# Optimization experiments

Measured on AMD Instinct MI355X. Metric: run time of the kernel, lower is better.

## Reference

```python
import jax, jax.numpy as jnp
import numpy as np

N = 50000      # nodes
DEG = 16       # in-degree per node -> E = 800k edges
IN = 256       # in_size
HID = 32       # hid_size
HEAD = 4       # heads in first layer
OUT = 40       # out_size (classes)
HH = HID * HEAD  # 128, hidden width
NEG_SLOPE = 0.2


def setup_inputs() -> dict:
    key = jax.random.key(0)
    ks = jax.random.split(key, 16)
    E = N * DEG
    src = jax.random.randint(ks[0], (E,), 0, N)
    dst = jnp.repeat(jnp.arange(N), DEG)  # every node has DEG in-edges

    def nrm(k, shape):
        return jax.random.normal(k, shape, jnp.float32) * 0.1

    return dict(
        features=jax.random.normal(ks[1], (N, IN), jnp.float32),
        src=src, dst=dst,
        # layer 1: GATConv(IN -> HID, HEAD heads)
        W1=nrm(ks[2], (IN, HH)), al1=nrm(ks[3], (HEAD, HID)), ar1=nrm(ks[4], (HEAD, HID)), b1=nrm(ks[5], (HH,)),
        # hidden layer: GATConv(HH -> HH, 1 head)
        Wh=nrm(ks[6], (HH, HH)), alh=nrm(ks[7], (1, HH)), arh=nrm(ks[8], (1, HH)), bh=nrm(ks[9], (HH,)),
        # layer 2: GATConv(HH -> OUT, 1 head)
        W2=nrm(ks[10], (HH, OUT)), al2=nrm(ks[11], (1, OUT)), ar2=nrm(ks[12], (1, OUT)), b2=nrm(ks[13], (OUT,)),
    )


def gat_conv(x, src, dst, W, al, ar, b):
    """DGL-style GATConv. x:[N,F], W:[F,H*D], al/ar:[H,D], b:[H*D]. Returns [N,H,D]."""
    n = x.shape[0]
    H, D = al.shape
    feat = (x @ W).reshape(n, H, D)                 # [N,H,D]
    el = jnp.sum(feat * al, axis=-1)                # [N,H]
    er = jnp.sum(feat * ar, axis=-1)                # [N,H]
    e = jax.nn.leaky_relu(el[src] + er[dst], NEG_SLOPE)  # [E,H] per-edge logits
    # segment softmax over each destination's in-edges
    emax = jax.lax.stop_gradient(jax.ops.segment_max(e, dst, num_segments=n))  # [N,H]
    ex = jnp.exp(e - emax[dst])                     # [E,H]
    den = jax.ops.segment_sum(ex, dst, num_segments=n)  # [N,H]
    alpha = ex / den[dst]                           # [E,H]
    out = jax.ops.segment_sum(feat[src] * alpha[:, :, None], dst, num_segments=n)  # [N,H,D]
    return out + b.reshape(1, H, D)


def reference(features, src, dst, W1, al1, ar1, b1, Wh, alh, arh, bh, W2, al2, ar2, b2):
    # conv1 -> flatten heads -> relu
    h = jax.nn.relu(gat_conv(features, src, dst, W1, al1, ar1, b1).reshape(N, HH))
    # hidden GATConv (1 head) -> mean over head -> relu (dropout is identity in eval)
    h = jax.nn.relu(gat_conv(h, src, dst, Wh, alh, arh, bh).mean(axis=1))
    # conv2 (1 head) -> mean over head -> log_softmax
    h = gat_conv(h, src, dst, W2, al2, ar2, b2).mean(axis=1)
    return jax.nn.log_softmax(h, axis=1)
```

## Files before the change

### kernel.cpp

```cpp
#include <hip/hip_runtime.h>
#include <cstddef>
#include <math.h>

#define NN 50000
#define DEG 16
#define NEG_SLOPE 0.2f

typedef __attribute__((ext_vector_type(8))) short bf16x8;
typedef __attribute__((ext_vector_type(4))) float f32x4;

__device__ inline unsigned short f2bf(float x) {
    unsigned u = __float_as_uint(x);
    return (unsigned short)((u + 0x7FFF + ((u >> 16) & 1)) >> 16);
}
__device__ inline float bf2f(unsigned short u) {
    return __uint_as_float(((unsigned)u) << 16);
}
__device__ inline unsigned pack_bf2(float lo, float hi) {
    return (unsigned)f2bf(lo) | ((unsigned)f2bf(hi) << 16);
}
__device__ inline void gld_lds16f(const float* g, float* l) {
    __builtin_amdgcn_global_load_lds((const __attribute__((address_space(1))) void*)g,
                                     (__attribute__((address_space(3))) void*)l, 16, 0, 0);
}

__global__ void prep_k(const float* __restrict__ W1, unsigned short* __restrict__ Wt1,
                       const float* __restrict__ Wh, unsigned short* __restrict__ Wth)
{
    const int b = blockIdx.x;
    if (b < 128) {
        int idx = b * 256 + threadIdx.x;
        int c = idx >> 8, k = idx & 255;
        Wt1[idx] = f2bf(W1[(size_t)k * 128 + c]);
    } else {
        int idx = (b - 128) * 256 + threadIdx.x;
        int c = idx >> 7, k = idx & 127;
        Wth[idx] = f2bf(Wh[(size_t)k * 128 + c]);
    }
}

__launch_bounds__(256)
__global__ void gemm1_k(const float* __restrict__ A,
                        const unsigned short* __restrict__ Wt,
                        const float* __restrict__ al, const float* __restrict__ ar,
                        unsigned short* __restrict__ feat,
                        float* __restrict__ el, float* __restrict__ er)
{
    constexpr int K = 256, KS = 8, TPB = 4;
    __shared__ __align__(16) float buf[2][4096];
    const int tid = threadIdx.x;
    const int w = tid >> 6, l = tid & 63;
    const int lr = l & 15, lq = l >> 4;
    const int col0 = w * 32;

    bf16x8 B0[KS], B1[KS];
#pragma unroll
    for (int ks = 0; ks < KS; ks++) {
        B0[ks] = *(const bf16x8*)(Wt + (size_t)(col0 + lr) * K + ks * 32 + lq * 8);
        B1[ks] = *(const bf16x8*)(Wt + (size_t)(col0 + 16 + lr) * K + ks * 32 + lq * 8);
    }

    const int t0 = blockIdx.x * TPB;
    const int tmax = NN / 16;
    const int t1 = (t0 + TPB < tmax) ? t0 + TPB : tmax;
    if (t0 >= tmax) return;

    auto stage = [&](int t, int b) {
#pragma unroll
        for (int p = 0; p < 4; p++) {
            int j = tid + p * 256;
            int row = j >> 6;
            int kg = (j & 63) ^ (row & 7);
            gld_lds16f(A + (size_t)(t * 16 + row) * 256 + kg * 4, &buf[b][(size_t)j * 4]);
        }
    };
    stage(t0, t0 & 1);

    for (int t = t0; t < t1; ++t) {
        __syncthreads();
        if (t + 1 < t1) stage(t + 1, (t + 1) & 1);

        f32x4 acc0 = {0.f, 0.f, 0.f, 0.f}, acc1 = {0.f, 0.f, 0.f, 0.f};
        const float* bb = buf[t & 1];
#pragma unroll
        for (int ks = 0; ks < KS; ks++) {
            const int kg0 = ks * 8 + lq * 2;
            const int s0 = lr * 64 + (kg0 ^ (lr & 7));
            const int s1 = lr * 64 + ((kg0 + 1) ^ (lr & 7));
            float4 va = *(const float4*)&bb[(size_t)s0 * 4];
            float4 vb = *(const float4*)&bb[(size_t)s1 * 4];
            bf16x8 a = {(short)f2bf(va.x), (short)f2bf(va.y),
                        (short)f2bf(va.z), (short)f2bf(va.w),
                        (short)f2bf(vb.x), (short)f2bf(vb.y),
                        (short)f2bf(vb.z), (short)f2bf(vb.w)};
            acc0 = __builtin_amdgcn_mfma_f32_16x16x32_bf16(a, B0[ks], acc0, 0, 0, 0);
            acc1 = __builtin_amdgcn_mfma_f32_16x16x32_bf16(a, B1[ks], acc1, 0, 0, 0);
        }

        const int row0 = t * 16;
#pragma unroll
        for (int reg = 0; reg < 4; reg++) {
            const int r = row0 + lq * 4 + reg;
            feat[(size_t)r * 128 + col0 + lr]      = f2bf(acc0[reg]);
            feat[(size_t)r * 128 + col0 + 16 + lr] = f2bf(acc1[reg]);
        }

        float pe[4], pr[4];
#pragma unroll
        for (int reg = 0; reg < 4; reg++) {
            pe[reg] = acc0[reg] * al[col0 + lr] + acc1[reg] * al[col0 + 16 + lr];
            pr[reg] = acc0[reg] * ar[col0 + lr] + acc1[reg] * ar[col0 + 16 + lr];
        }
#pragma unroll
        for (int m = 1; m < 16; m <<= 1)
#pragma unroll
            for (int reg = 0; reg < 4; reg++) {
                pe[reg] += __shfl_xor(pe[reg], m);
                pr[reg] += __shfl_xor(pr[reg], m);
            }
        if (lr == 0) {
#pragma unroll
            for (int reg = 0; reg < 4; reg++) {
                const int r = row0 + lq * 4 + reg;
                el[r * 4 + w] = pe[reg];
                er[r * 4 + w] = pr[reg];
            }
        }
    }
}

__launch_bounds__(256)
__global__ void fusedh_k(const unsigned short* __restrict__ feat1,
                         const float* __restrict__ el1, const float* __restrict__ er1,
                         const int* __restrict__ src, const float* __restrict__ b1,
                         const unsigned short* __restrict__ Wt,
                         const float* __restrict__ alh, const float* __restrict__ arh,
                         unsigned short* __restrict__ feat2,
                         float* __restrict__ el, float* __restrict__ er)
{
    __shared__ __align__(16) unsigned short abuf[256 * 8];
    __shared__ float s_alpha[16][64];
    __shared__ float redE[4][16], redR[4][16];
    const int tid = threadIdx.x;
    const int w = tid >> 6, lane = tid & 63;
    const int q = lane >> 4, li = lane & 15;
    const int slot = w * 4 + q;
    const int row0 = blockIdx.x * 16;
    const int node = row0 + slot;
    const int col0 = w * 32;

    const int s = src[node * DEG + li];
    {
        const float4 elv = *(const float4*)(el1 + (size_t)s * 4);
        const float4 erv = *(const float4*)(er1 + (size_t)node * 4);
        float e[4] = {elv.x + erv.x, elv.y + erv.y, elv.z + erv.z, elv.w + erv.w};
#pragma unroll
        for (int h = 0; h < 4; h++) {
            float x = e[h];
            x = (x > 0.f) ? x : NEG_SLOPE * x;
            float mx = x;
#pragma unroll
            for (int d = 1; d < 16; d <<= 1) mx = fmaxf(mx, __shfl_xor(mx, d, 16));
            float ex = expf(x - mx);
            float den = ex;
#pragma unroll
            for (int d = 1; d < 16; d <<= 1) den += __shfl_xor(den, d, 16);
            s_alpha[slot][h * 16 + li] = ex / den;
        }
    }
    uint4 v[16];
#pragma unroll
    for (int jj = 0; jj < 16; jj++) {
        int sj = __shfl(s, (lane & 48) | jj);
        v[jj] = *(const uint4*)(feat1 + (size_t)sj * 128 + li * 8);
    }
    float acc[8] = {0.f, 0.f, 0.f, 0.f, 0.f, 0.f, 0.f, 0.f};
    const int hrow = (li >> 2) * 16;
#pragma unroll
    for (int jj = 0; jj < 16; jj++) {
        float a = s_alpha[slot][hrow + jj];
        unsigned u0 = v[jj].x, u1 = v[jj].y, u2 = v[jj].z, u3 = v[jj].w;
        acc[0] += a * bf2f((unsigned short)(u0 & 0xFFFF));
        acc[1] += a * bf2f((unsigned short)(u0 >> 16));
        acc[2] += a * bf2f((unsigned short)(u1 & 0xFFFF));
        acc[3] += a * bf2f((unsigned short)(u1 >> 16));
        acc[4] += a * bf2f((unsigned short)(u2 & 0xFFFF));
        acc[5] += a * bf2f((unsigned short)(u2 >> 16));
        acc[6] += a * bf2f((unsigned short)(u3 & 0xFFFF));
        acc[7] += a * bf2f((unsigned short)(u3 >> 16));
    }
    const float4 bb0 = *(const float4*)(b1 + li * 8);
    const float4 bb1 = *(const float4*)(b1 + li * 8 + 4);
    float o[8];
    o[0] = fmaxf(acc[0] + bb0.x, 0.f); o[1] = fmaxf(acc[1] + bb0.y, 0.f);
    o[2] = fmaxf(acc[2] + bb0.z, 0.f); o[3] = fmaxf(acc[3] + bb0.w, 0.f);
    o[4] = fmaxf(acc[4] + bb1.x, 0.f); o[5] = fmaxf(acc[5] + bb1.y, 0.f);
    o[6] = fmaxf(acc[6] + bb1.z, 0.f); o[7] = fmaxf(acc[7] + bb1.w, 0.f);
    {
        uint4 pk;
        pk.x = pack_bf2(o[0], o[1]);
        pk.y = pack_bf2(o[2], o[3]);
        pk.z = pack_bf2(o[4], o[5]);
        pk.w = pack_bf2(o[6], o[7]);
        int jw = ((li >> 2) * 64 + (li & 3) * 16 + slot) ^ (li & 7);
        *(uint4*)&abuf[(size_t)jw * 8] = pk;
    }

    bf16x8 B0[4], B1[4];
#pragma unroll
    for (int ks = 0; ks < 4; ks++) {
        B0[ks] = *(const bf16x8*)(Wt + (size_t)(col0 + li) * 128 + ks * 32 + q * 8);
        B1[ks] = *(const bf16x8*)(Wt + (size_t)(col0 + 16 + li) * 128 + ks * 32 + q * 8);
    }
    __syncthreads();

    f32x4 acc0 = {0.f, 0.f, 0.f, 0.f}, acc1 = {0.f, 0.f, 0.f, 0.f};
#pragma unroll
    for (int ks = 0; ks < 4; ks++) {
        int jr = (ks * 64 + lane) ^ ((ks * 4 + q) & 7);
        bf16x8 a = *(const bf16x8*)&abuf[(size_t)jr * 8];
        acc0 = __builtin_amdgcn_mfma_f32_16x16x32_bf16(a, B0[ks], acc0, 0, 0, 0);
        acc1 = __builtin_amdgcn_mfma_f32_16x16x32_bf16(a, B1[ks], acc1, 0, 0, 0);
    }

#pragma unroll
    for (int reg = 0; reg < 4; reg++) {
        const int r = row0 + q * 4 + reg;
        feat2[(size_t)r * 128 + col0 + li]      = f2bf(acc0[reg]);
        feat2[(size_t)r * 128 + col0 + 16 + li] = f2bf(acc1[reg]);
    }
    float pe[4], pr[4];
#pragma unroll
    for (int reg = 0; reg < 4; reg++) {
        pe[reg] = acc0[reg] * alh[col0 + li] + acc1[reg] * alh[col0 + 16 + li];
        pr[reg] = acc0[reg] * arh[col0 + li] + acc1[reg] * arh[col0 + 16 + li];
    }
#pragma unroll
    for (int m = 1; m < 16; m <<= 1)
#pragma unroll
        for (int reg = 0; reg < 4; reg++) {
            pe[reg] += __shfl_xor(pe[reg], m);
            pr[reg] += __shfl_xor(pr[reg], m);
        }
    if (li == 0) {
#pragma unroll
        for (int reg = 0; reg < 4; reg++) {
            redE[w][q * 4 + reg] = pe[reg];
            redR[w][q * 4 + reg] = pr[reg];
        }
    }
    __syncthreads();
    if (tid < 16) {
        el[row0 + tid] = redE[0][tid] + redE[1][tid] + redE[2][tid] + redE[3][tid];
        er[row0 + tid] = redR[0][tid] + redR[1][tid] + redR[2][tid] + redR[3][tid];
    }
}

__launch_bounds__(256)
__global__ void fused40_k(const unsigned short* __restrict__ feat2,
                          const float* __restrict__ elA, const float* __restrict__ erA,
                          const int* __restrict__ src, const float* __restrict__ bh,
                          const float* __restrict__ W2,
                          const float* __restrict__ al2, const float* __restrict__ ar2,
                          unsigned short* __restrict__ f40,
                          float* __restrict__ el2, float* __restrict__ er2)
{
    __shared__ float As[32][132];
    __shared__ float Ws[128 * 40];
    const int tid = threadIdx.x;
    const int w = tid >> 6, lane = tid & 63;
    const int q = lane >> 4, li = lane & 15;
    const int slot = w * 4 + q;
    const int row0 = blockIdx.x * 32;

#pragma unroll
    for (int rnd = 0; rnd < 2; rnd++) {
        const int row = rnd * 16 + slot;
        int node = row0 + row;
        if (node > NN - 1) node = NN - 1;
        const int s = src[node * DEG + li];
        float x = elA[s] + erA[node];
        x = (x > 0.f) ? x : NEG_SLOPE * x;
        float mx = x;
#pragma unroll
        for (int d = 1; d < 16; d <<= 1) mx = fmaxf(mx, __shfl_xor(mx, d, 16));
        float ex = expf(x - mx);
        float den = ex;
#pragma unroll
        for (int d = 1; d < 16; d <<= 1) den += __shfl_xor(den, d, 16);
        const float alpha = ex / den;

        uint4 v[16];
#pragma unroll
        for (int jj = 0; jj < 16; jj++) {
            int sj = __shfl(s, (lane & 48) | jj);
            v[jj] = *(const uint4*)(feat2 + (size_t)sj * 128 + li * 8);
        }
        float acc[8] = {0.f, 0.f, 0.f, 0.f, 0.f, 0.f, 0.f, 0.f};
#pragma unroll
        for (int jj = 0; jj < 16; jj++) {
            float a = __shfl(alpha, (lane & 48) | jj);
            unsigned u0 = v[jj].x, u1 = v[jj].y, u2 = v[jj].z, u3 = v[jj].w;
            acc[0] += a * bf2f((unsigned short)(u0 & 0xFFFF));
            acc[1] += a * bf2f((unsigned short)(u0 >> 16));
            acc[2] += a * bf2f((unsigned short)(u1 & 0xFFFF));
            acc[3] += a * bf2f((unsigned short)(u1 >> 16));
            acc[4] += a * bf2f((unsigned short)(u2 & 0xFFFF));
            acc[5] += a * bf2f((unsigned short)(u2 >> 16));
            acc[6] += a * bf2f((unsigned short)(u3 & 0xFFFF));
            acc[7] += a * bf2f((unsigned short)(u3 >> 16));
        }
        const float4 bb0 = *(const float4*)(bh + li * 8);
        const float4 bb1 = *(const float4*)(bh + li * 8 + 4);
        float4 o0, o1;
        o0.x = fmaxf(acc[0] + bb0.x, 0.f); o0.y = fmaxf(acc[1] + bb0.y, 0.f);
        o0.z = fmaxf(acc[2] + bb0.z, 0.f); o0.w = fmaxf(acc[3] + bb0.w, 0.f);
        o1.x = fmaxf(acc[4] + bb1.x, 0.f); o1.y = fmaxf(acc[5] + bb1.y, 0.f);
        o1.z = fmaxf(acc[6] + bb1.z, 0.f); o1.w = fmaxf(acc[7] + bb1.w, 0.f);
        *(float4*)&As[row][li * 8]     = o0;
        *(float4*)&As[row][li * 8 + 4] = o1;
    }
    {
        const float4* s4 = (const float4*)W2;
        float4* d4 = (float4*)Ws;
#pragma unroll
        for (int p = 0; p < 5; p++) d4[tid + 256 * p] = s4[tid + 256 * p];
    }
    __syncthreads();

    const int tx = tid & 31;
    const int ty = tid >> 5;
    const int ctx = (tx < 20) ? tx : 19;
    const float2* Wf2 = (const float2*)Ws;
    float acc[4][2] = {};
#pragma unroll 4
    for (int k = 0; k < 128; k++) {
        float2 wv = Wf2[k * 20 + ctx];
#pragma unroll
        for (int i = 0; i < 4; i++) {
            float a = As[ty * 4 + i][k];
            acc[i][0] += a * wv.x;
            acc[i][1] += a * wv.y;
        }
    }
    float pel[4], per[4];
#pragma unroll
    for (int i = 0; i < 4; i++) {
        float vl = 0.f, vr = 0.f;
        if (tx < 20) {
            vl = acc[i][0] * al2[2 * ctx] + acc[i][1] * al2[2 * ctx + 1];
            vr = acc[i][0] * ar2[2 * ctx] + acc[i][1] * ar2[2 * ctx + 1];
        }
        pel[i] = vl; per[i] = vr;
    }
#pragma unroll
    for (int m = 1; m < 32; m <<= 1) {
#pragma unroll
        for (int i = 0; i < 4; i++) {
            pel[i] += __shfl_xor(pel[i], m);
            per[i] += __shfl_xor(per[i], m);
        }
    }
#pragma unroll
    for (int i = 0; i < 4; i++) {
        int r = row0 + ty * 4 + i;
        if (r < NN) {
            if (tx < 20) *(unsigned*)&f40[(size_t)r * 40 + 2 * tx] = pack_bf2(acc[i][0], acc[i][1]);
            if (tx == 0) { el2[r] = pel[i]; er2[r] = per[i]; }
        }
    }
}

__launch_bounds__(256)
__global__ void agg40_ls_k(const unsigned short* __restrict__ feat, const float* __restrict__ el,
                           const float* __restrict__ er, const int* __restrict__ src,
                           const float* __restrict__ bias, float* __restrict__ out)
{
    const int tid = threadIdx.x;
    const int w = tid >> 6, lane = tid & 63;
    const int half = lane >> 5, li = lane & 31;
    const int node = blockIdx.x * 8 + w * 2 + half;

    const int s = src[node * DEG + (li & 15)];
    float e = el[s] + er[node];
    e = (e > 0.f) ? e : NEG_SLOPE * e;
    float mx = e;
#pragma unroll
    for (int d = 1; d < 16; d <<= 1) mx = fmaxf(mx, __shfl_xor(mx, d, 16));
    float ex = expf(e - mx);
    float den = ex;
#pragma unroll
    for (int d = 1; d < 16; d <<= 1) den += __shfl_xor(den, d, 16);
    const float alpha = ex / den;

    const int cli = (li < 20) ? li : 19;
    float acc0 = 0.f, acc1 = 0.f;
#pragma unroll
    for (int jj = 0; jj < DEG; jj++) {
        int sj = __shfl(s, jj, 32);
        float a = __shfl(alpha, jj, 32);
        unsigned v = *(const unsigned*)(feat + (size_t)sj * 40 + 2 * cli);
        acc0 += a * bf2f((unsigned short)(v & 0xFFFF));
        acc1 += a * bf2f((unsigned short)(v >> 16));
    }
    float v0 = acc0 + bias[2 * cli], v1 = acc1 + bias[2 * cli + 1];
    float m2 = (li < 20) ? fmaxf(v0, v1) : -INFINITY;
#pragma unroll
    for (int d = 1; d < 32; d <<= 1) m2 = fmaxf(m2, __shfl_xor(m2, d, 32));
    float pe = (li < 20) ? (expf(v0 - m2) + expf(v1 - m2)) : 0.f;
    float se = pe;
#pragma unroll
    for (int d = 1; d < 32; d <<= 1) se += __shfl_xor(se, d, 32);
    if (li < 20) {
        float ls = m2 + logf(se);
        out[(size_t)node * 40 + 2 * li]     = v0 - ls;
        out[(size_t)node * 40 + 2 * li + 1] = v1 - ls;
    }
}

extern "C" void kernel_launch(void* const* d_in, const int* in_sizes, int n_in,
                              void* d_out, int out_size, void* d_ws, size_t ws_size,
                              hipStream_t stream)
{
    const float* features = (const float*)d_in[0];
    const int*   src      = (const int*)d_in[1];
    const float* W1  = (const float*)d_in[3];
    const float* al1 = (const float*)d_in[4];
    const float* ar1 = (const float*)d_in[5];
    const float* b1  = (const float*)d_in[6];
    const float* Wh  = (const float*)d_in[7];
    const float* alh = (const float*)d_in[8];
    const float* arh = (const float*)d_in[9];
    const float* bh  = (const float*)d_in[10];
    const float* W2  = (const float*)d_in[11];
    const float* al2 = (const float*)d_in[12];
    const float* ar2 = (const float*)d_in[13];
    const float* b2  = (const float*)d_in[14];
    float* out = (float*)d_out;

    float* ws = (float*)d_ws;
    unsigned short* featb  = (unsigned short*)ws;
    unsigned short* featb2 = featb + (size_t)NN * 128;
    float* el1  = (float*)(featb2 + (size_t)NN * 128);
    float* er1  = el1 + (size_t)NN * 4;
    float* elA  = er1 + (size_t)NN * 4;
    float* erA  = elA + NN;
    float* el2  = erA + NN;
    float* er2  = el2 + NN;
    unsigned short* f40b = (unsigned short*)(er2 + NN);
    unsigned short* Wt1  = f40b + (size_t)NN * 40;
    unsigned short* Wth  = Wt1 + 128 * 256;

    dim3 blk(256);
    prep_k<<<192, blk, 0, stream>>>(W1, Wt1, Wh, Wth);
    gemm1_k<<<782, blk, 0, stream>>>(features, Wt1, al1, ar1, featb, el1, er1);
    fusedh_k<<<3125, blk, 0, stream>>>(featb, el1, er1, src, b1, Wth, alh, arh,
                                       featb2, elA, erA);
    fused40_k<<<1563, blk, 0, stream>>>(featb2, elA, erA, src, bh, W2, al2, ar2,
                                        f40b, el2, er2);
    agg40_ls_k<<<6250, blk, 0, stream>>>(f40b, el2, er2, src, b2, out);
}
```

Baseline: 119.9 us.

## Stage neighbor feature gathers through LDS via direct global-to-LDS loads

Replaces the per-lane register gather of 16 neighbor feature rows in the hidden and final aggregation kernels with global_load_lds copies into a per-wave swizzled LDS buffer, done in two halves of 8 neighbors. The first half is issued before the softmax computation so the gather latency can overlap it. The aim is to cut register pressure from holding 16 uint4 values per lane, which should help occupancy. In exchange it adds 32 KB of shared memory per block, which may limit occupancy on its own, plus explicit waitcnt serialization between the two halves.

```diff
diff --git a/kernel.cpp b/kernel.cpp
--- a/kernel.cpp
+++ b/kernel.cpp
@@ -23,6 +23,43 @@
     __builtin_amdgcn_global_load_lds((const __attribute__((address_space(1))) void*)g,
                                      (__attribute__((address_space(3))) void*)l, 16, 0, 0);
 }
+__device__ inline void gld_lds16u(const unsigned short* g, unsigned short* l) {
+    __builtin_amdgcn_global_load_lds((const __attribute__((address_space(1))) void*)g,
+                                     (__attribute__((address_space(3))) void*)l, 16, 0, 0);
+}
+
+#define STAGE_HALF(gb, sv, feat, hf)                                          \
+    {                                                                          \
+        _Pragma("unroll")                                                      \
+        for (int i = 0; i < 8; i++) {                                          \
+            int nl = i >> 1;                                                   \
+            int jjh = (i & 1) * 4 + (lane >> 4);                               \
+            int sj = __shfl(sv, nl * 16 + (hf) * 8 + jjh);                     \
+            int gc = (lane & 15) ^ (nl << 1);                                  \
+            gld_lds16u((feat) + (size_t)sj * 128 + gc * 8,                     \
+                       (gb) + i * 512 + lane * 8);                             \
+        }                                                                      \
+    }
+
+#define ACC_HALF(gb, hf, ALPHA)                                               \
+    {                                                                          \
+        _Pragma("unroll")                                                      \
+        for (int jjh = 0; jjh < 8; jjh++) {                                    \
+            int jj = (hf) * 8 + jjh;                                           \
+            float a = (ALPHA);                                                 \
+            uint4 v = *(const uint4*)&(gb)[q * 1024 + jjh * 128 +              \
+                                           ((li ^ (q << 1)) * 8)];             \
+            unsigned u0 = v.x, u1 = v.y, u2 = v.z, u3 = v.w;                   \
+            acc[0] += a * bf2f((unsigned short)(u0 & 0xFFFF));                 \
+            acc[1] += a * bf2f((unsigned short)(u0 >> 16));                    \
+            acc[2] += a * bf2f((unsigned short)(u1 & 0xFFFF));                 \
+            acc[3] += a * bf2f((unsigned short)(u1 >> 16));                    \
+            acc[4] += a * bf2f((unsigned short)(u2 & 0xFFFF));                 \
+            acc[5] += a * bf2f((unsigned short)(u2 >> 16));                    \
+            acc[6] += a * bf2f((unsigned short)(u3 & 0xFFFF));                 \
+            acc[7] += a * bf2f((unsigned short)(u3 >> 16));                    \
+        }                                                                      \
+    }
 
 __global__ void prep_k(const float* __restrict__ W1, unsigned short* __restrict__ Wt1,
                        const float* __restrict__ Wh, unsigned short* __restrict__ Wth)
@@ -138,6 +175,7 @@
                          unsigned short* __restrict__ feat2,
                          float* __restrict__ el, float* __restrict__ er)
 {
+    __shared__ __align__(16) unsigned short gbuf[4][4096];
     __shared__ __align__(16) unsigned short abuf[256 * 8];
     __shared__ float s_alpha[16][64];
     __shared__ float redE[4][16], redR[4][16];
@@ -148,8 +186,13 @@
     const int row0 = blockIdx.x * 16;
     const int node = row0 + slot;
     const int col0 = w * 32;
-
-    const int s = src[node * DEG + li];
+    unsigned short* gb = &gbuf[w][0];
+
+    const int sv = src[(size_t)(row0 + w * 4) * 16 + lane];
+    const int s = sv;
+
+    STAGE_HALF(gb, sv, feat1, 0);
+
     {
         const float4 elv = *(const float4*)(el1 + (size_t)s * 4);
         const float4 erv = *(const float4*)(er1 + (size_t)node * 4);
@@ -168,27 +211,16 @@
             s_alpha[slot][h * 16 + li] = ex / den;
         }
     }
-    uint4 v[16];
-#pragma unroll
-    for (int jj = 0; jj < 16; jj++) {
-        int sj = __shfl(s, (lane & 48) | jj);
-        v[jj] = *(const uint4*)(feat1 + (size_t)sj * 128 + li * 8);
-    }
+
+    const int hrow = (li >> 2) * 16;
     float acc[8] = {0.f, 0.f, 0.f, 0.f, 0.f, 0.f, 0.f, 0.f};
-    const int hrow = (li >> 2) * 16;
-#pragma unroll
-    for (int jj = 0; jj < 16; jj++) {
-        float a = s_alpha[slot][hrow + jj];
-        unsigned u0 = v[jj].x, u1 = v[jj].y, u2 = v[jj].z, u3 = v[jj].w;
-        acc[0] += a * bf2f((unsigned short)(u0 & 0xFFFF));
-        acc[1] += a * bf2f((unsigned short)(u0 >> 16));
-        acc[2] += a * bf2f((unsigned short)(u1 & 0xFFFF));
-        acc[3] += a * bf2f((unsigned short)(u1 >> 16));
-        acc[4] += a * bf2f((unsigned short)(u2 & 0xFFFF));
-        acc[5] += a * bf2f((unsigned short)(u2 >> 16));
-        acc[6] += a * bf2f((unsigned short)(u3 & 0xFFFF));
-        acc[7] += a * bf2f((unsigned short)(u3 >> 16));
-    }
+    asm volatile("s_waitcnt vmcnt(0)" ::: "memory");
+    ACC_HALF(gb, 0, s_alpha[slot][hrow + jj]);
+    asm volatile("s_waitcnt lgkmcnt(0)" ::: "memory");
+    STAGE_HALF(gb, sv, feat1, 1);
+    asm volatile("s_waitcnt vmcnt(0)" ::: "memory");
+    ACC_HALF(gb, 1, s_alpha[slot][hrow + jj]);
+
     const float4 bb0 = *(const float4*)(b1 + li * 8);
     const float4 bb1 = *(const float4*)(b1 + li * 8 + 4);
     float o[8];
@@ -265,6 +297,7 @@
                           unsigned short* __restrict__ f40,
                           float* __restrict__ el2, float* __restrict__ er2)
 {
+    __shared__ __align__(16) unsigned short gbuf[4][4096];
     __shared__ float As[32][132];
     __shared__ float Ws[128 * 40];
     const int tid = threadIdx.x;
@@ -272,14 +305,19 @@
     const int q = lane >> 4, li = lane & 15;
     const int slot = w * 4 + q;
     const int row0 = blockIdx.x * 32;
+    unsigned short* gb = &gbuf[w][0];
 
 #pragma unroll
     for (int rnd = 0; rnd < 2; rnd++) {
-        const int row = rnd * 16 + slot;
-        int node = row0 + row;
-        if (node > NN - 1) node = NN - 1;
-        const int s = src[node * DEG + li];
-        float x = elA[s] + erA[node];
+        const int nb = row0 + rnd * 16;
+        int myn = nb + w * 4 + (lane >> 4); if (myn > NN - 1) myn = NN - 1;
+        const int sv = src[(size_t)myn * 16 + (lane & 15)];
+        const int s = sv;
+        int nodeq = nb + slot; if (nodeq > NN - 1) nodeq = NN - 1;
+
+        STAGE_HALF(gb, sv, feat2, 0);
+
+        float x = elA[s] + erA[nodeq];
         x = (x > 0.f) ? x : NEG_SLOPE * x;
         float mx = x;
 #pragma unroll
@@ -290,26 +328,14 @@
         for (int d = 1; d < 16; d <<= 1) den += __shfl_xor(den, d, 16);
         const float alpha = ex / den;
 
-        uint4 v[16];
-#pragma unroll
-        for (int jj = 0; jj < 16; jj++) {
-            int sj = __shfl(s, (lane & 48) | jj);
-            v[jj] = *(const uint4*)(feat2 + (size_t)sj * 128 + li * 8);
-        }
         float acc[8] = {0.f, 0.f, 0.f, 0.f, 0.f, 0.f, 0.f, 0.f};
-#pragma unroll
-        for (int jj = 0; jj < 16; jj++) {
-            float a = __shfl(alpha, (lane & 48) | jj);
-            unsigned u0 = v[jj].x, u1 = v[jj].y, u2 = v[jj].z, u3 = v[jj].w;
-            acc[0] += a * bf2f((unsigned short)(u0 & 0xFFFF));
-            acc[1] += a * bf2f((unsigned short)(u0 >> 16));
-            acc[2] += a * bf2f((unsigned short)(u1 & 0xFFFF));
-            acc[3] += a * bf2f((unsigned short)(u1 >> 16));
-            acc[4] += a * bf2f((unsigned short)(u2 & 0xFFFF));
-            acc[5] += a * bf2f((unsigned short)(u2 >> 16));
-            acc[6] += a * bf2f((unsigned short)(u3 & 0xFFFF));
-            acc[7] += a * bf2f((unsigned short)(u3 >> 16));
-        }
+        asm volatile("s_waitcnt vmcnt(0)" ::: "memory");
+        ACC_HALF(gb, 0, __shfl(alpha, (lane & 48) | jj));
+        asm volatile("s_waitcnt lgkmcnt(0)" ::: "memory");
+        STAGE_HALF(gb, sv, feat2, 1);
+        asm volatile("s_waitcnt vmcnt(0)" ::: "memory");
+        ACC_HALF(gb, 1, __shfl(alpha, (lane & 48) | jj));
+
         const float4 bb0 = *(const float4*)(bh + li * 8);
         const float4 bb1 = *(const float4*)(bh + li * 8 + 4);
         float4 o0, o1;
@@ -317,6 +343,7 @@
         o0.z = fmaxf(acc[2] + bb0.z, 0.f); o0.w = fmaxf(acc[3] + bb0.w, 0.f);
         o1.x = fmaxf(acc[4] + bb1.x, 0.f); o1.y = fmaxf(acc[5] + bb1.y, 0.f);
         o1.z = fmaxf(acc[6] + bb1.z, 0.f); o1.w = fmaxf(acc[7] + bb1.w, 0.f);
+        const int row = rnd * 16 + slot;
         *(float4*)&As[row][li * 8]     = o0;
         *(float4*)&As[row][li * 8 + 4] = o1;
     }
```

Measured after the change: 139.8 us. 16.6% more time.
